# Kernel optimization log

Hardware: AMD Instinct MI355X
Metric: run time of the kernel (lower is better)

## Reference

```python
import jax, jax.numpy as jnp
import numpy as np
from jax import lax

B, C, H0, W0 = 8, 128, 62, 62
G, K, DIL, STRIDE, PAD = 4, 3, 1, 1, 1
P = K * K
GC = C // G
OFFSET_SCALE = 1.0


def setup_inputs() -> dict:
    key = jax.random.key(0)
    ks = jax.random.split(key, 10)
    s = 0.05
    return {
        "x": jax.random.normal(ks[0], (B, C, H0, W0), jnp.float32),
        "conv_w": jax.random.normal(ks[1], (C, C, 1, 1), jnp.float32) * s,
        "conv_b": jax.random.normal(ks[2], (C,), jnp.float32) * s,
        "in_proj_w": jax.random.normal(ks[3], (C, C), jnp.float32) * s,
        "in_proj_b": jnp.zeros((C,), jnp.float32),
        "dw_w": jax.random.normal(ks[4], (C, 1, K, K), jnp.float32) * s,
        "dw_b": jnp.zeros((C,), jnp.float32),
        "ln_g": jnp.ones((C,), jnp.float32),
        "ln_b": jnp.zeros((C,), jnp.float32),
        "off_w": jax.random.normal(ks[5], (C, G * P * 2), jnp.float32) * s,
        "off_b": jax.random.normal(ks[6], (G * P * 2,), jnp.float32) * s,
        "mask_w": jax.random.normal(ks[7], (C, G * P), jnp.float32) * s,
        "mask_b": jnp.zeros((G * P,), jnp.float32),
        "out_proj_w": jax.random.normal(ks[8], (C, C), jnp.float32) * s,
        "out_proj_b": jnp.zeros((C,), jnp.float32),
    }


def _bilinear_sample(img, ix, iy, Hp, Wp):
    # img: [B, G, Hp*Wp, GC] flattened spatial; ix, iy: [B, G, Q, P] pixel coords.
    # Matches torch grid_sample(bilinear, zeros, align_corners=False).
    x0 = jnp.floor(ix)
    y0 = jnp.floor(iy)

    def gather(xi, yi):
        valid = (xi >= 0) & (xi <= Wp - 1) & (yi >= 0) & (yi <= Hp - 1)
        xc = jnp.clip(xi, 0, Wp - 1).astype(jnp.int32)
        yc = jnp.clip(yi, 0, Hp - 1).astype(jnp.int32)
        lin = (yc * Wp + xc).reshape(img.shape[0], img.shape[1], -1)  # [B,G,Q*P]
        v = jnp.take_along_axis(img, lin[..., None], axis=2)          # [B,G,Q*P,GC]
        v = v.reshape(xi.shape + (img.shape[-1],))
        return v * valid[..., None].astype(img.dtype)

    wx1 = (ix - x0)[..., None]
    wx0 = 1.0 - wx1
    wy1 = (iy - y0)[..., None]
    wy0 = 1.0 - wy1
    return (gather(x0, y0) * wx0 * wy0
            + gather(x0 + 1.0, y0) * wx1 * wy0
            + gather(x0, y0 + 1.0) * wx0 * wy1
            + gather(x0 + 1.0, y0 + 1.0) * wx1 * wy1)


def _dcnv3_core(x_proj, offset, mask):
    # x_proj: [B,H,W,C] NHWC; offset: [B,H,W,G*P*2]; mask: [B,H,W,G*P] (softmaxed)
    Bn, H, W, _ = x_proj.shape
    xp = jnp.pad(x_proj, ((0, 0), (PAD, PAD), (PAD, PAD), (0, 0)))
    Hp, Wp = H + 2 * PAD, W + 2 * PAD  # H_out == H for K=3, PAD=1, STRIDE=1
    # reference points (normalized to padded size)
    ref_x = (jnp.arange(W, dtype=jnp.float32) * STRIDE + (DIL * (K - 1)) / 2.0 + 0.5) / Wp
    ref_y = (jnp.arange(H, dtype=jnp.float32) * STRIDE + (DIL * (K - 1)) / 2.0 + 0.5) / Hp
    ref = jnp.stack(jnp.broadcast_arrays(ref_x[None, :], ref_y[:, None]), -1)  # [H,W,2] (x,y)
    # dilation grid (same ordering as torch.meshgrid(x_lin, y_lin))
    klin = (jnp.arange(K, dtype=jnp.float32) * DIL - (DIL * (K - 1)) // 2)
    gx, gy = jnp.meshgrid(klin, klin, indexing='ij')
    grid = jnp.stack([gx / Wp, gy / Hp], -1).reshape(P, 2)
    grid = jnp.tile(grid[None], (G, 1, 1)).reshape(G * P, 2)
    spatial_norm = jnp.array([Wp, Hp], jnp.float32)
    loc = (ref[:, :, None, :] + grid[None, None] * OFFSET_SCALE)[None] \
        + offset.reshape(Bn, H, W, G * P, 2) * OFFSET_SCALE / spatial_norm
    g = 2.0 * loc - 1.0  # normalized grid in [-1,1]
    ix = ((g[..., 0] + 1.0) * Wp - 1.0) / 2.0  # align_corners=False unnormalize
    iy = ((g[..., 1] + 1.0) * Hp - 1.0) / 2.0
    Q = H * W
    ix = ix.reshape(Bn, Q, G, P).transpose(0, 2, 1, 3)  # [B,G,Q,P]
    iy = iy.reshape(Bn, Q, G, P).transpose(0, 2, 1, 3)
    img = xp.reshape(Bn, Hp * Wp, G, GC).transpose(0, 2, 1, 3)  # [B,G,S,GC]
    sampled = _bilinear_sample(img, ix, iy, Hp, Wp)             # [B,G,Q,P,GC]
    m = mask.reshape(Bn, Q, G, P).transpose(0, 2, 1, 3)
    out = jnp.einsum('bgqpc,bgqp->bqgc', sampled, m)
    return out.reshape(Bn, H, W, G * GC)


def reference(x, conv_w, conv_b, in_proj_w, in_proj_b, dw_w, dw_b, ln_g, ln_b,
              off_w, off_b, mask_w, mask_b, out_proj_w, out_proj_b):
    dn = ('NCHW', 'OIHW', 'NCHW')
    # 1x1 conv with padding=1 (spatial grows by 2 on each dim)
    y = lax.conv_general_dilated(x, conv_w, (1, 1), ((PAD, PAD), (PAD, PAD)),
                                 dimension_numbers=dn) + conv_b[None, :, None, None]
    t = y.transpose(0, 2, 3, 1)  # NHWC
    x_proj = t @ in_proj_w + in_proj_b
    # offset/mask branch: depthwise conv + LayerNorm + GELU
    d = lax.conv_general_dilated(y, dw_w, (1, 1), ((1, 1), (1, 1)),
                                 dimension_numbers=dn,
                                 feature_group_count=C) + dw_b[None, :, None, None]
    d = d.transpose(0, 2, 3, 1)
    mu = d.mean(-1, keepdims=True)
    var = ((d - mu) ** 2).mean(-1, keepdims=True)
    d = (d - mu) / jnp.sqrt(var + 1e-5) * ln_g + ln_b
    d = jax.nn.gelu(d, approximate=False)
    offset = d @ off_w + off_b
    Bn, H, W, _ = d.shape
    m = jax.nn.softmax((d @ mask_w + mask_b).reshape(Bn, H, W, G, P), axis=-1)
    out = _dcnv3_core(x_proj, offset, m.reshape(Bn, H, W, G * P))
    out = out @ out_proj_w + out_proj_b
    return out.transpose(0, 3, 1, 2)  # back to NCHW
```

## Files before the change

### kernel.cpp

```cpp
#include <hip/hip_runtime.h>
#include <math.h>

#define BB 8
#define CH 128
#define HH 64
#define WWID 64
#define HIN 62
#define WIN 62
#define SPIN (HIN*WIN)
#define HP 66
#define WP 66
#define GP2 70
#define GG 4
#define GCH 32
#define NPIX (BB*HH*WWID)
#define ASTRIDE 136

typedef _Float16 v8h __attribute__((ext_vector_type(8)));
typedef _Float16 v4h __attribute__((ext_vector_type(4)));
typedef float    v4f __attribute__((ext_vector_type(4)));
typedef float    f4a __attribute__((ext_vector_type(4), aligned(4)));

__global__ __launch_bounds__(256) void p0_pack(const float* __restrict__ conv_w,
                                               const float* __restrict__ in_proj_w,
                                               const float* __restrict__ off_w,
                                               const float* __restrict__ mask_w,
                                               const float* __restrict__ out_proj_w,
                                               const float* __restrict__ dw_w,
                                               _Float16* __restrict__ wp,
                                               float* __restrict__ dwT) {
    int t = threadIdx.x;
    if (blockIdx.x == 31) {
        if (t < 128) {
            #pragma unroll
            for (int tap = 0; tap < 9; tap++) dwT[tap * 128 + t] = dw_w[t * 9 + tap];
        }
        return;
    }
    int tid = blockIdx.x * 256 + t;
    int mat, base;
    if (tid < 2048)      { mat = 0; base = 0; }
    else if (tid < 4096) { mat = 1; base = 2048; }
    else if (tid < 5888) { mat = 2; base = 4096; }
    else                 { mat = 3; base = 5888; }
    int fi = tid - base;
    int nt = fi >> 8, rem = fi & 255, kc = rem >> 6, lane = rem & 63;
    int n = nt * 16 + (lane & 15);
    int kbase = kc * 32 + ((lane >> 4) & 3) * 8;
    _Float16* dst = wp + (size_t)tid * 8;
    #pragma unroll
    for (int j = 0; j < 8; j++) {
        int k = kbase + j;
        float v;
        if (mat == 0)      v = conv_w[n * CH + k];
        else if (mat == 1) v = in_proj_w[k * CH + n];
        else if (mat == 2) v = (n < 72) ? off_w[k * 72 + n]
                               : (n < 108 ? mask_w[k * 36 + (n - 72)] : 0.f);
        else               v = out_proj_w[k * CH + n];
        dst[j] = (_Float16)v;
    }
}

__device__ inline void mfma_loop8(const _Float16* __restrict__ a16,
                                  const _Float16* __restrict__ wp,
                                  v4f acc[4], int t) {
    int lane = t & 63;
    int wv = t >> 6;
    int mt = wv >> 1, ntb = (wv & 1) * 4;
    const _Float16* abase = a16 + (mt * 16 + (lane & 15)) * ASTRIDE + ((lane >> 4) * 8);
    #pragma unroll
    for (int kc = 0; kc < 4; kc++) {
        v8h av = *(const v8h*)(abase + kc * 32);
        #pragma unroll
        for (int j = 0; j < 4; j++) {
            v8h bv = *(const v8h*)(wp + ((size_t)((ntb + j) * 4 + kc) * 64 + lane) * 8);
            acc[j] = __builtin_amdgcn_mfma_f32_16x16x32_f16(av, bv, acc[j], 0, 0, 0);
        }
    }
}

__device__ inline void acc_to_a16_8(_Float16* a16, v4f acc[4], int t) {
    int lane = t & 63, ncol = lane & 15;
    int wv = t >> 6;
    int m0 = (wv >> 1) * 16 + ((lane >> 4) * 4);
    int ntb = (wv & 1) * 4;
    #pragma unroll
    for (int j = 0; j < 4; j++)
        #pragma unroll
        for (int r = 0; r < 4; r++)
            a16[(m0 + r) * ASTRIDE + (ntb + j) * 16 + ncol] = (_Float16)acc[j][r];
}

__global__ __launch_bounds__(512) void gA_conv_inproj(const float* __restrict__ x,
                                                      const _Float16* __restrict__ wp_conv,
                                                      const _Float16* __restrict__ wp_in,
                                                      const float* __restrict__ conv_b,
                                                      const float* __restrict__ in_b,
                                                      _Float16* __restrict__ y16,
                                                      _Float16* __restrict__ xpad16) {
    __shared__ _Float16 a16[64 * ASTRIDE];
    int pix0 = blockIdx.x * 64;
    int t = threadIdx.x;
    int h = (pix0 >> 6) & 63, b = pix0 >> 12;
    bool hin = (h >= 1 && h <= 62);
    for (int q = t; q < 2048; q += 512) {
        int c = q >> 4, w4 = (q & 15) * 4;
        float4 v = make_float4(0.f, 0.f, 0.f, 0.f);
        if (hin) {
            const float* xr = x + ((size_t)(b * CH + c)) * SPIN + (h - 1) * WIN;
            if (w4 == 0)       { f4a e = *(const f4a*)&xr[0];      v = make_float4(0.f, e[0], e[1], e[2]); }
            else if (w4 == 60) { f4a e = *(const f4a*)&xr[58];     v = make_float4(e[1], e[2], e[3], 0.f); }
            else               { f4a e = *(const f4a*)&xr[w4 - 1]; v = make_float4(e[0], e[1], e[2], e[3]); }
        }
        a16[(w4 + 0) * ASTRIDE + c] = (_Float16)v.x;
        a16[(w4 + 1) * ASTRIDE + c] = (_Float16)v.y;
        a16[(w4 + 2) * ASTRIDE + c] = (_Float16)v.z;
        a16[(w4 + 3) * ASTRIDE + c] = (_Float16)v.w;
    }
    __syncthreads();
    int lane = t & 63, ncol = lane & 15;
    int ntb = ((t >> 6) & 1) * 4;
    v4f acc[4];
    #pragma unroll
    for (int j = 0; j < 4; j++) {
        float bv = conv_b[(ntb + j) * 16 + ncol];
        acc[j] = (v4f){bv, bv, bv, bv};
    }
    mfma_loop8(a16, wp_conv, acc, t);
    __syncthreads();
    acc_to_a16_8(a16, acc, t);
    __syncthreads();
    {
        _Float16* dst = y16 + (size_t)pix0 * CH;
        for (int q = t; q < 1024; q += 512)
            *(v8h*)&dst[q * 8] = *(const v8h*)&a16[(q >> 4) * ASTRIDE + (q & 15) * 8];
    }
    v4f acc2[4];
    #pragma unroll
    for (int j = 0; j < 4; j++) {
        float bv = in_b[(ntb + j) * 16 + ncol];
        acc2[j] = (v4f){bv, bv, bv, bv};
    }
    mfma_loop8(a16, wp_in, acc2, t);
    __syncthreads();
    acc_to_a16_8(a16, acc2, t);
    __syncthreads();
    {
        _Float16* dst = xpad16 + (size_t)(((b * GP2) + h + 3) * GP2 + 3) * CH;
        for (int q = t; q < 1024; q += 512)
            *(v8h*)&dst[q * 8] = *(const v8h*)&a16[(q >> 4) * ASTRIDE + (q & 15) * 8];
    }
}

__global__ __launch_bounds__(512) void gF_dwln_offmask(const _Float16* __restrict__ y16,
                                                       const _Float16* __restrict__ wp_om,
                                                       const float* __restrict__ dwT,
                                                       const float* __restrict__ dw_b,
                                                       const float* __restrict__ ln_g,
                                                       const float* __restrict__ ln_b,
                                                       const float* __restrict__ off_b,
                                                       const float* __restrict__ mask_b,
                                                       float* __restrict__ tapmeta) {
    __shared__ char smem[49920];
    _Float16* ylds = (_Float16*)smem;
    int t = threadIdx.x;
    int pix0 = blockIdx.x * 64;
    int h = (pix0 >> 6) & 63, b = pix0 >> 12;
    if (h == 0 || h == 63) {
        for (int i = t; i < 3120; i += 512) *(v8h*)&ylds[i * 8] = (v8h)(_Float16)0;
        __syncthreads();
    }
    for (int idx = t; idx < 3072; idx += 512) {
        int r = idx >> 10, w = (idx >> 4) & 63, c8 = idx & 15;
        int hh = h + r - 1;
        if (hh >= 0 && hh <= 63) {
            v8h v = *(const v8h*)&y16[(size_t)(((b * 64 + hh) * 64 + w) * CH) + c8 * 8];
            *(v8h*)&ylds[(size_t)((r * 16 + c8) * 65 + w) * 8] = v;
        }
    }
    __syncthreads();
    int px = t >> 3, q8 = t & 7;
    float acc[16];
    #pragma unroll
    for (int cb = 0; cb < 4; cb++) *(float4*)&acc[cb * 4] = *(const float4*)&dw_b[q8 * 16 + cb * 4];
    #pragma unroll
    for (int r = 0; r < 3; r++) {
        #pragma unroll
        for (int kx = 0; kx < 3; kx++) {
            int wq = px + kx - 1;
            bool valid = (wq >= 0 && wq <= 63);
            int wpc = min(max(wq, 0), 63);
            int tap = r * 3 + kx;
            if (valid) {
                #pragma unroll
                for (int cb = 0; cb < 2; cb++) {
                    v8h yv = *(const v8h*)&ylds[(size_t)((r * 16 + q8 * 2 + cb) * 65 + wpc) * 8];
                    float4 wa = *(const float4*)&dwT[tap * 128 + q8 * 16 + cb * 8];
                    float4 wb = *(const float4*)&dwT[tap * 128 + q8 * 16 + cb * 8 + 4];
                    acc[cb*8+0] += (float)yv[0] * wa.x; acc[cb*8+1] += (float)yv[1] * wa.y;
                    acc[cb*8+2] += (float)yv[2] * wa.z; acc[cb*8+3] += (float)yv[3] * wa.w;
                    acc[cb*8+4] += (float)yv[4] * wb.x; acc[cb*8+5] += (float)yv[5] * wb.y;
                    acc[cb*8+6] += (float)yv[6] * wb.z; acc[cb*8+7] += (float)yv[7] * wb.w;
                }
            }
        }
    }
    float s = 0.f, ss = 0.f;
    #pragma unroll
    for (int j = 0; j < 16; j++) { s += acc[j]; ss += acc[j] * acc[j]; }
    s  += __shfl_xor(s, 1);  s  += __shfl_xor(s, 2);  s  += __shfl_xor(s, 4);
    ss += __shfl_xor(ss, 1); ss += __shfl_xor(ss, 2); ss += __shfl_xor(ss, 4);
    float mu = s * (1.f / 128.f);
    float var = ss * (1.f / 128.f) - mu * mu;
    float rstd = rsqrtf(var + 1e-5f);
    v8h dreg[2];
    #pragma unroll
    for (int cb = 0; cb < 2; cb++) {
        float4 ga = *(const float4*)&ln_g[q8 * 16 + cb * 8];
        float4 gb = *(const float4*)&ln_g[q8 * 16 + cb * 8 + 4];
        float4 ba = *(const float4*)&ln_b[q8 * 16 + cb * 8];
        float4 bb = *(const float4*)&ln_b[q8 * 16 + cb * 8 + 4];
        float gv[8] = {ga.x, ga.y, ga.z, ga.w, gb.x, gb.y, gb.z, gb.w};
        float bv[8] = {ba.x, ba.y, ba.z, ba.w, bb.x, bb.y, bb.z, bb.w};
        #pragma unroll
        for (int j = 0; j < 8; j++) {
            float xln = (acc[cb * 8 + j] - mu) * rstd * gv[j] + bv[j];
            float gel = 0.5f * xln * (1.f + erff(xln * 0.70710678118654752f));
            dreg[cb][j] = (_Float16)gel;
        }
    }
    __syncthreads();
    _Float16* a16 = (_Float16*)smem;
    float* om = (float*)(smem + 17408);
    #pragma unroll
    for (int cb = 0; cb < 2; cb++)
        *(v8h*)&a16[px * ASTRIDE + q8 * 16 + cb * 8] = dreg[cb];
    __syncthreads();
    int lane = t & 63, ncol = lane & 15;
    int ntb = ((t >> 6) & 1) * 4;
    v4f macc[4];
    #pragma unroll
    for (int j = 0; j < 4; j++) {
        int n = (ntb + j) * 16 + ncol;
        float bv = (n < 72) ? off_b[n] : (n < 108 ? mask_b[n - 72] : 0.f);
        macc[j] = (v4f){bv, bv, bv, bv};
    }
    mfma_loop8(a16, wp_om, macc, t);
    int m0 = ((t >> 6) >> 1) * 16 + ((lane >> 4) * 4);
    #pragma unroll
    for (int j = 0; j < 4; j++) {
        if (ntb + j < 7) {
            #pragma unroll
            for (int r = 0; r < 4; r++)
                om[(m0 + r) * 112 + (ntb + j) * 16 + ncol] = macc[j][r];
        }
    }
    __syncthreads();
    if (t < 256) {
        int pxs = t >> 2, gx = t & 3;
        const float* row = &om[pxs * 112];
        float lg[9];
        #pragma unroll
        for (int i = 0; i < 9; i++) lg[i] = row[72 + gx * 9 + i];
        float mx = lg[0];
        #pragma unroll
        for (int i = 1; i < 9; i++) mx = fmaxf(mx, lg[i]);
        float e[9], sum = 0.f;
        #pragma unroll
        for (int i = 0; i < 9; i++) { e[i] = expf(lg[i] - mx); sum += e[i]; }
        float inv = 1.f / sum;
        float* tm = tapmeta + ((size_t)(pix0 + pxs) * 36 + gx * 9) * 4;
        #pragma unroll
        for (int p = 0; p < 9; p++) {
            int gp = gx * 9 + p;
            float offx = row[gp * 2];
            float offy = row[gp * 2 + 1];
            float m = e[p] * inv;
            float ix = (float)(pxs + (p / 3)) + offx;
            float iy = (float)(h + (p % 3)) + offy;
            ix = fminf(fmaxf(ix, -2.f), (float)(WP + 1));
            iy = fminf(fmaxf(iy, -2.f), (float)(HP + 1));
            float x0f = floorf(ix), y0f = floorf(iy);
            float fx = ix - x0f, fy = iy - y0f;
            int x0 = (int)x0f, y0 = (int)y0f;
            int off = ((y0 + 2) * GP2 + (x0 + 2)) * CH;
            float4 rec;
            rec.x = __int_as_float(off);
            rec.y = fx; rec.z = fy; rec.w = m;
            *(float4*)&tm[p * 4] = rec;
        }
    }
}

__global__ __launch_bounds__(256) void kD_gather(const _Float16* __restrict__ xpad16,
                                                 const float* __restrict__ tapmeta,
                                                 _Float16* __restrict__ core16) {
    __shared__ float meta[8 * 36 * 4];
    int t = threadIdx.x;
    int pix0 = blockIdx.x * 8;
    const float4* src = (const float4*)(tapmeta + (size_t)pix0 * 36 * 4);
    for (int i = t; i < 288; i += 256) ((float4*)meta)[i] = src[i];
    __syncthreads();
    int px_l = t >> 5, lane5 = t & 31;
    int c4 = lane5 * 4, g = lane5 >> 3;
    int pix = pix0 + px_l;
    int b = pix >> 12;
    const _Float16* base = xpad16 + (size_t)b * GP2 * GP2 * CH + c4;
    float a0 = 0.f, a1 = 0.f, a2 = 0.f, a3 = 0.f;
    #pragma unroll
    for (int p = 0; p < 9; p++) {
        float4 rec = *(const float4*)&meta[(size_t)(px_l * 36 + g * 9 + p) * 4];
        int off = __float_as_int(rec.x);
        float fx = rec.y, fy = rec.z, m = rec.w;
        float w11 = fx * fy;
        float w10 = fx - w11;
        float w01 = fy - w11;
        float w00 = 1.f - fx - fy + w11;
        w00 *= m; w10 *= m; w01 *= m; w11 *= m;
        v4h h0 = *(const v4h*)&base[off];
        v4h h1 = *(const v4h*)&base[off + CH];
        v4h h2 = *(const v4h*)&base[off + GP2 * CH];
        v4h h3 = *(const v4h*)&base[off + GP2 * CH + CH];
        a0 += w00*(float)h0[0] + w10*(float)h1[0] + w01*(float)h2[0] + w11*(float)h3[0];
        a1 += w00*(float)h0[1] + w10*(float)h1[1] + w01*(float)h2[1] + w11*(float)h3[1];
        a2 += w00*(float)h0[2] + w10*(float)h1[2] + w01*(float)h2[2] + w11*(float)h3[2];
        a3 += w00*(float)h0[3] + w10*(float)h1[3] + w01*(float)h2[3] + w11*(float)h3[3];
    }
    v4h res = { (_Float16)a0, (_Float16)a1, (_Float16)a2, (_Float16)a3 };
    *(v4h*)&core16[(size_t)pix * CH + c4] = res;
}

__global__ __launch_bounds__(512) void g4_outproj(const _Float16* __restrict__ core16,
                                                  const _Float16* __restrict__ wp,
                                                  const float* __restrict__ bias,
                                                  float* __restrict__ out) {
    __shared__ _Float16 a16[64 * ASTRIDE];
    __shared__ float res[64 * 129];
    int pix0 = blockIdx.x * 64;
    int t = threadIdx.x;
    const _Float16* src = core16 + (size_t)pix0 * CH;
    for (int q = t; q < 1024; q += 512)
        *(v8h*)&a16[(q >> 4) * ASTRIDE + (q & 15) * 8] = *(const v8h*)&src[q * 8];
    __syncthreads();
    int lane = t & 63, ncol = lane & 15;
    int ntb = ((t >> 6) & 1) * 4;
    v4f acc[4];
    #pragma unroll
    for (int j = 0; j < 4; j++) {
        float bv = bias[(ntb + j) * 16 + ncol];
        acc[j] = (v4f){bv, bv, bv, bv};
    }
    mfma_loop8(a16, wp, acc, t);
    int m0 = ((t >> 6) >> 1) * 16 + ((lane >> 4) * 4);
    #pragma unroll
    for (int j = 0; j < 4; j++)
        #pragma unroll
        for (int r = 0; r < 4; r++)
            res[(m0 + r) * 129 + (ntb + j) * 16 + ncol] = acc[j][r];
    __syncthreads();
    int b = pix0 >> 12, h = (pix0 >> 6) & 63;
    for (int q = t; q < 2048; q += 512) {
        int cc = q >> 4, w4 = (q & 15) * 4;
        float4 o;
        o.x = res[(w4 + 0) * 129 + cc];
        o.y = res[(w4 + 1) * 129 + cc];
        o.z = res[(w4 + 2) * 129 + cc];
        o.w = res[(w4 + 3) * 129 + cc];
        *(float4*)&out[(size_t)((b * CH + cc) * HH + h) * WWID + w4] = o;
    }
}

extern "C" void kernel_launch(void* const* d_in, const int* in_sizes, int n_in,
                              void* d_out, int out_size, void* d_ws, size_t ws_size,
                              hipStream_t stream) {
    const float* x        = (const float*)d_in[0];
    const float* conv_w   = (const float*)d_in[1];
    const float* conv_b   = (const float*)d_in[2];
    const float* in_proj_w= (const float*)d_in[3];
    const float* in_proj_b= (const float*)d_in[4];
    const float* dw_w     = (const float*)d_in[5];
    const float* dw_b     = (const float*)d_in[6];
    const float* ln_g     = (const float*)d_in[7];
    const float* ln_b     = (const float*)d_in[8];
    const float* off_w    = (const float*)d_in[9];
    const float* off_b    = (const float*)d_in[10];
    const float* mask_w   = (const float*)d_in[11];
    const float* mask_b   = (const float*)d_in[12];
    const float* out_proj_w = (const float*)d_in[13];
    const float* out_proj_b = (const float*)d_in[14];
    float* out = (float*)d_out;

    float* ws = (float*)d_ws;
    const size_t O_WP   = 0;
    const size_t O_DWT  = 32768;
    const size_t O_Y16  = 34816;
    const size_t O_XP16 = O_Y16 + 2097152;
    const size_t O_C16  = O_XP16 + 2508800;
    const size_t O_TM   = O_C16 + 2097152;
    _Float16* wp     = (_Float16*)(ws + O_WP);
    float*    dwT    = ws + O_DWT;
    _Float16* y16    = (_Float16*)(ws + O_Y16);
    _Float16* xpad16 = (_Float16*)(ws + O_XP16);
    _Float16* core16 = (_Float16*)(ws + O_C16);
    float*    tapmeta= ws + O_TM;

    _Float16* wp_conv = wp;
    _Float16* wp_in   = wp + (size_t)2048 * 8;
    _Float16* wp_om   = wp + (size_t)4096 * 8;
    _Float16* wp_out  = wp + (size_t)5888 * 8;

    p0_pack<<<32, 256, 0, stream>>>(conv_w, in_proj_w, off_w, mask_w, out_proj_w, dw_w, wp, dwT);
    hipMemsetAsync(xpad16, 0, (size_t)8 * GP2 * GP2 * CH * sizeof(_Float16), stream);
    gA_conv_inproj<<<NPIX / 64, 512, 0, stream>>>(x, wp_conv, wp_in, conv_b, in_proj_b, y16, xpad16);
    gF_dwln_offmask<<<NPIX / 64, 512, 0, stream>>>(y16, wp_om, dwT, dw_b, ln_g, ln_b, off_b, mask_b, tapmeta);
    kD_gather<<<NPIX / 8, 256, 0, stream>>>(xpad16, tapmeta, core16);
    g4_outproj<<<NPIX / 64, 512, 0, stream>>>(core16, wp_out, out_proj_b, out);
}
```

Baseline: 165.6 us.

## Fold xpad zeroing into pack kernel, split tap metadata work, transpose outproj staging

The separate hipMemsetAsync on the padded input buffer is replaced by 32 extra blocks in the weight-pack kernel that zero it with vector stores, removing one launch. In the offset/mask kernel all 512 threads now build tap metadata, with each (pixel, group) job split across two threads handling 5 and 4 taps; this duplicates the softmax computation but halves per-thread serial work. The out-projection staging buffer is transposed to channel-major with stride 68, so the NCHW writeback reads one float4 instead of four strided scalars, at the cost of possible bank conflicts on the MFMA result stores.

```diff
diff --git a/kernel.cpp b/kernel.cpp
--- a/kernel.cpp
+++ b/kernel.cpp
@@ -15,6 +15,7 @@
 #define GCH 32
 #define NPIX (BB*HH*WWID)
 #define ASTRIDE 136
+#define XPHALFS ((size_t)BB*GP2*GP2*CH)
 
 typedef _Float16 v8h __attribute__((ext_vector_type(8)));
 typedef _Float16 v4h __attribute__((ext_vector_type(4)));
@@ -28,16 +29,24 @@
                                                const float* __restrict__ out_proj_w,
                                                const float* __restrict__ dw_w,
                                                _Float16* __restrict__ wp,
-                                               float* __restrict__ dwT) {
+                                               float* __restrict__ dwT,
+                                               _Float16* __restrict__ xpad16) {
     int t = threadIdx.x;
-    if (blockIdx.x == 31) {
+    int blk = blockIdx.x;
+    if (blk >= 32) {
+        size_t nvec = XPHALFS / 8;
+        for (size_t i = (size_t)(blk - 32) * 256 + t; i < nvec; i += 32 * 256)
+            *(v8h*)&xpad16[i * 8] = (v8h)(_Float16)0;
+        return;
+    }
+    if (blk == 31) {
         if (t < 128) {
             #pragma unroll
             for (int tap = 0; tap < 9; tap++) dwT[tap * 128 + t] = dw_w[t * 9 + tap];
         }
         return;
     }
-    int tid = blockIdx.x * 256 + t;
+    int tid = blk * 256 + t;
     int mat, base;
     if (tid < 2048)      { mat = 0; base = 0; }
     else if (tid < 4096) { mat = 1; base = 2048; }
@@ -256,8 +265,9 @@
         }
     }
     __syncthreads();
-    if (t < 256) {
-        int pxs = t >> 2, gx = t & 3;
+    {
+        int job = t >> 1, half = t & 1;
+        int pxs = job >> 2, gx = job & 3;
         const float* row = &om[pxs * 112];
         float lg[9];
         #pragma unroll
@@ -270,8 +280,12 @@
         for (int i = 0; i < 9; i++) { e[i] = expf(lg[i] - mx); sum += e[i]; }
         float inv = 1.f / sum;
         float* tm = tapmeta + ((size_t)(pix0 + pxs) * 36 + gx * 9) * 4;
-        #pragma unroll
-        for (int p = 0; p < 9; p++) {
+        int pstart = half * 5;
+        int pcount = half ? 4 : 5;
+        #pragma unroll
+        for (int pp = 0; pp < 5; pp++) {
+            if (pp >= pcount) break;
+            int p = pstart + pp;
             int gp = gx * 9 + p;
             float offx = row[gp * 2];
             float offy = row[gp * 2 + 1];
@@ -335,7 +349,7 @@
                                                   const float* __restrict__ bias,
                                                   float* __restrict__ out) {
     __shared__ _Float16 a16[64 * ASTRIDE];
-    __shared__ float res[64 * 129];
+    __shared__ float res[128 * 68];
     int pix0 = blockIdx.x * 64;
     int t = threadIdx.x;
     const _Float16* src = core16 + (size_t)pix0 * CH;
@@ -356,16 +370,12 @@
     for (int j = 0; j < 4; j++)
         #pragma unroll
         for (int r = 0; r < 4; r++)
-            res[(m0 + r) * 129 + (ntb + j) * 16 + ncol] = acc[j][r];
+            res[((ntb + j) * 16 + ncol) * 68 + (m0 + r)] = acc[j][r];
     __syncthreads();
     int b = pix0 >> 12, h = (pix0 >> 6) & 63;
     for (int q = t; q < 2048; q += 512) {
         int cc = q >> 4, w4 = (q & 15) * 4;
-        float4 o;
-        o.x = res[(w4 + 0) * 129 + cc];
-        o.y = res[(w4 + 1) * 129 + cc];
-        o.z = res[(w4 + 2) * 129 + cc];
-        o.w = res[(w4 + 3) * 129 + cc];
+        float4 o = *(const float4*)&res[cc * 68 + w4];
         *(float4*)&out[(size_t)((b * CH + cc) * HH + h) * WWID + w4] = o;
     }
 }
@@ -409,8 +419,7 @@
     _Float16* wp_om   = wp + (size_t)4096 * 8;
     _Float16* wp_out  = wp + (size_t)5888 * 8;
 
-    p0_pack<<<32, 256, 0, stream>>>(conv_w, in_proj_w, off_w, mask_w, out_proj_w, dw_w, wp, dwT);
-    hipMemsetAsync(xpad16, 0, (size_t)8 * GP2 * GP2 * CH * sizeof(_Float16), stream);
+    p0_pack<<<64, 256, 0, stream>>>(conv_w, in_proj_w, off_w, mask_w, out_proj_w, dw_w, wp, dwT, xpad16);
     gA_conv_inproj<<<NPIX / 64, 512, 0, stream>>>(x, wp_conv, wp_in, conv_b, in_proj_b, y16, xpad16);
     gF_dwln_offmask<<<NPIX / 64, 512, 0, stream>>>(y16, wp_om, dwT, dw_b, ln_g, ln_b, off_b, mask_b, tapmeta);
     kD_gather<<<NPIX / 8, 256, 0, stream>>>(xpad16, tapmeta, core16);
```

New measurement: 162.7 us. No clear change (-1.8%).
